# Kernel tuning notes

Hardware: AMD Instinct MI355X
Metric: run time of the kernel (lower is better)

Reference implementation:

```python
import jax, jax.numpy as jnp
import numpy as np

EPS = 1e-7  # keras.backend.epsilon()
CANONICAL_SIZE = 224.0
CANONICAL_LEVEL = 1.0
MIN_LEVEL, MAX_LEVEL = 0, 4


def _crop_and_resize(feat, boxes, crop_h, crop_w):
    """TF crop_and_resize (bilinear, extrapolation_value=0) for one image.
    feat: [H, W, C]; boxes: [N, 4] normalized (y1, x1, y2, x2).
    Returns [N, crop_h, crop_w, C]."""
    H, W, C = feat.shape
    hf = jnp.asarray(H - 1, feat.dtype)
    wf = jnp.asarray(W - 1, feat.dtype)
    y1, x1, y2, x2 = boxes[:, 0], boxes[:, 1], boxes[:, 2], boxes[:, 3]
    ty = jnp.arange(crop_h, dtype=feat.dtype) / (crop_h - 1)  # [ch]
    tx = jnp.arange(crop_w, dtype=feat.dtype) / (crop_w - 1)  # [cw]
    ys = (y1[:, None] + (y2 - y1)[:, None] * ty[None, :]) * hf  # [N, ch]
    xs = (x1[:, None] + (x2 - x1)[:, None] * tx[None, :]) * wf  # [N, cw]
    valid_y = (ys >= 0) & (ys <= hf)
    valid_x = (xs >= 0) & (xs <= wf)
    y0 = jnp.floor(ys)
    x0 = jnp.floor(xs)
    ly = ys - y0  # lerp weights [N, ch]
    lx = xs - x0  # [N, cw]
    y0i = jnp.clip(y0, 0, H - 1).astype(jnp.int32)
    y1i = jnp.clip(y0 + 1, 0, H - 1).astype(jnp.int32)
    x0i = jnp.clip(x0, 0, W - 1).astype(jnp.int32)
    x1i = jnp.clip(x0 + 1, 0, W - 1).astype(jnp.int32)
    # gather 4 corners -> [N, ch, cw, C]
    f00 = feat[y0i[:, :, None], x0i[:, None, :]]
    f01 = feat[y0i[:, :, None], x1i[:, None, :]]
    f10 = feat[y1i[:, :, None], x0i[:, None, :]]
    f11 = feat[y1i[:, :, None], x1i[:, None, :]]
    wy = ly[:, :, None, None]
    wx = lx[:, None, :, None]
    top = f00 + (f01 - f00) * wx
    bot = f10 + (f11 - f10) * wx
    out = top + (bot - top) * wy
    valid = (valid_y[:, :, None] & valid_x[:, None, :])[..., None]
    return jnp.where(valid, out, jnp.zeros((), feat.dtype))


def _map_to_level(boxes):
    w = boxes[:, 2] - boxes[:, 0]
    h = boxes[:, 3] - boxes[:, 1]
    size = jnp.sqrt(w * h)
    levels = jnp.floor(CANONICAL_LEVEL + jnp.log2(size / CANONICAL_SIZE + EPS))
    return jnp.clip(levels, MIN_LEVEL, MAX_LEVEL).astype(jnp.int32)


def roi_align(detections, fpn, top_k=1000, crop_size=(14, 14)):
    det = detections[0]                       # [N, 4+num_classes]
    scores = jnp.max(det[:, 4:], axis=1)      # [N]
    _, idx = jax.lax.top_k(scores, top_k)
    det = det[idx]                            # [K, 4+nc]
    levels = _map_to_level(det[:, :4])        # [K]
    # original concatenates level-0 rois, then level-1, ... == stable sort by level
    order = jnp.argsort(levels, stable=True)
    det = det[order]
    levels = levels[order]
    ch, cw = crop_size
    C = fpn[0].shape[-1]
    out = jnp.zeros((top_k, ch, cw, C), fpn[0].dtype)
    for i, f in enumerate(fpn):
        feat = f[0]                           # [H, W, C]
        H, W = feat.shape[0], feat.shape[1]
        hf = jnp.asarray(H - 1, feat.dtype)
        wf = jnp.asarray(W - 1, feat.dtype)
        boxes = jnp.stack([det[:, 1] / hf, det[:, 0] / wf,
                           det[:, 3] / hf, det[:, 2] / wf], axis=1)
        crops = _crop_and_resize(feat, boxes, ch, cw)
        out = jnp.where((levels == i)[:, None, None, None], crops, out)
    return out[None]                          # [1, K, ch, cw, C]


def setup_inputs() -> dict:
    key = jax.random.key(0)
    ks = jax.random.split(key, 10)
    N, NC = 5000, 80
    cx = jax.random.uniform(ks[0], (N,)) * 1024.0
    cy = jax.random.uniform(ks[1], (N,)) * 1024.0
    size = jnp.exp2(jax.random.uniform(ks[2], (N,)) * 5.0 + 5.0)   # 32..1024
    ar = jnp.exp2(jax.random.uniform(ks[3], (N,)) * 2.0 - 1.0)     # 0.5..2
    w = size * jnp.sqrt(ar)
    h = size / jnp.sqrt(ar)
    x1 = jnp.maximum(cx - w / 2, 0.0)
    y1 = jnp.maximum(cy - h / 2, 0.0)
    x2 = x1 + w
    y2 = y1 + h
    cls = jax.random.uniform(ks[4], (N, NC))
    detections = jnp.concatenate(
        [jnp.stack([x1, y1, x2, y2], axis=1), cls], axis=1)[None]  # [1,N,84]
    C = 256
    shapes = [256, 128, 64, 32, 16]
    fpn = {f"p{i}": jax.random.normal(ks[5 + i], (1, s, s, C), jnp.float32)
           for i, s in enumerate(shapes)}
    return {"detections": detections, **fpn}


def reference(detections, p0, p1, p2, p3, p4):
    return roi_align(detections, [p0, p1, p2, p3, p4],
                     top_k=1000, crop_size=(14, 14))
```

## Files before the change

kernel.cpp:

```cpp
#include <hip/hip_runtime.h>

#define NDET 5000
#define NCLS 80
#define DSTR 84
#define TOPK 1000
#define CROP 14
#define NPIX (CROP * CROP)
#define C    256

#define JCHUNK 250
#define ICHUNK 256

typedef float v4f __attribute__((ext_vector_type(4)));

__global__ void scores_kernel(const float* __restrict__ det, float* __restrict__ scores,
                              int* __restrict__ rank, int* __restrict__ lvl_all) {
    int i = blockIdx.x * blockDim.x + threadIdx.x;
    if (i >= NDET) return;
    const float* row = det + i * DSTR;
    const v4f* cls = (const v4f*)(row + 4);
    v4f m4 = cls[0];
    #pragma unroll
    for (int c = 1; c < NCLS / 4; ++c) {
        v4f v = cls[c];
        m4.x = fmaxf(m4.x, v.x); m4.y = fmaxf(m4.y, v.y);
        m4.z = fmaxf(m4.z, v.z); m4.w = fmaxf(m4.w, v.w);
    }
    scores[i] = fmaxf(fmaxf(m4.x, m4.y), fmaxf(m4.z, m4.w));
    rank[i] = 0;
    float w = row[2] - row[0];
    float h = row[3] - row[1];
    float sz = sqrtf(w * h);
    float lf = floorf(1.0f + log2f(sz / 224.0f + 1e-7f));
    lf = fminf(fmaxf(lf, 0.0f), 4.0f);
    lvl_all[i] = (int)lf;
}

__global__ __launch_bounds__(ICHUNK) void rank_kernel(const float* __restrict__ scores,
                                                      int* __restrict__ rank) {
    __shared__ float s[JCHUNK];
    int jbase = blockIdx.y * JCHUNK;
    for (int t = threadIdx.x; t < JCHUNK; t += blockDim.x) s[t] = scores[jbase + t];
    __syncthreads();
    int i = blockIdx.x * ICHUNK + threadIdx.x;
    if (i >= NDET) return;
    float my = scores[i];
    int r = 0;
    #pragma unroll 5
    for (int t = 0; t < JCHUNK; ++t) {
        float v = s[t];
        int j = jbase + t;
        r += (v > my) | ((v == my) & (j < i));
    }
    atomicAdd(&rank[i], r);
}

__global__ __launch_bounds__(1024) void order_kernel(const float* __restrict__ det,
                                                     const int* __restrict__ rank,
                                                     const int* __restrict__ lvl_all,
                                                     v4f* __restrict__ slot_params,
                                                     int* __restrict__ slot_level) {
    __shared__ int topk_idx_s[TOPK];
    __shared__ unsigned long long wave_tot[16];
    int r = threadIdx.x;
    for (int i = r; i < NDET; i += 1024) {
        int rk = rank[i];
        if (rk < TOPK) topk_idx_s[rk] = i;
    }
    __syncthreads();

    int di = 0, L = 0;
    unsigned long long key = 0;
    if (r < TOPK) {
        di = topk_idx_s[r];
        L = lvl_all[di];
        key = 1ULL << (12 * L);
    }
    unsigned long long incl = key;
    #pragma unroll
    for (int d = 1; d < 64; d <<= 1) {
        unsigned long long up = __shfl_up(incl, d, 64);
        if ((r & 63) >= d) incl += up;
    }
    int wave = r >> 6;
    if ((r & 63) == 63) wave_tot[wave] = incl;
    __syncthreads();
    unsigned long long waveoff = 0, total = 0;
    for (int w = 0; w < 16; ++w) {
        unsigned long long t = wave_tot[w];
        if (w < wave) waveoff += t;
        total += t;
    }
    if (r < TOPK) {
        unsigned long long excl = waveoff + incl - key;
        int base = 0;
        for (int l = 0; l < L; ++l) base += (int)((total >> (12 * l)) & 0xFFF);
        int within = (int)((excl >> (12 * L)) & 0xFFF);
        int pos = base + within;
        int H = 256 >> L;
        float hf = (float)(H - 1);
        const float* b = det + di * DSTR;
        float x1n = b[0] / hf, y1n = b[1] / hf;
        float x2n = b[2] / hf, y2n = b[3] / hf;
        v4f prm = {x1n, y1n, x2n - x1n, y2n - y1n};
        slot_params[pos] = prm;
        slot_level[pos] = L;
    }
}

__global__ __launch_bounds__(256) void crop_kernel(
    const float* __restrict__ p0, const float* __restrict__ p1,
    const float* __restrict__ p2, const float* __restrict__ p3,
    const float* __restrict__ p4,
    const v4f* __restrict__ slot_params, const int* __restrict__ slot_level,
    float* __restrict__ out)
{
    int wave = threadIdx.x >> 6;
    int lane = threadIdx.x & 63;
    int slot = blockIdx.x / 49;
    int p    = (blockIdx.x % 49) * 4 + wave;
    int py = p / CROP, px = p - py * CROP;

    int L = slot_level[slot];
    const float* feat;
    switch (L) {
        case 0:  feat = p0; break;
        case 1:  feat = p1; break;
        case 2:  feat = p2; break;
        case 3:  feat = p3; break;
        default: feat = p4; break;
    }
    int H = 256 >> L;
    float hf = (float)(H - 1);

    v4f prm = slot_params[slot];
    float ty = (float)py / 13.0f;
    float tx = (float)px / 13.0f;
    float ys = (prm.y + prm.w * ty) * hf;
    float xs = (prm.x + prm.z * tx) * hf;

    v4f* outp = (v4f*)(out + (size_t)(slot * NPIX + p) * C) + lane;

    bool valid = (ys >= 0.0f) & (ys <= hf) & (xs >= 0.0f) & (xs <= hf);
    if (!valid) {
        v4f z = {0.0f, 0.0f, 0.0f, 0.0f};
        *outp = z;
        return;
    }

    float y0f = floorf(ys), x0f = floorf(xs);
    float ly = ys - y0f,    lx = xs - x0f;
    int y0i = (int)fminf(fmaxf(y0f,        0.0f), hf);
    int y1i = (int)fminf(fmaxf(y0f + 1.0f, 0.0f), hf);
    int x0i = (int)fminf(fmaxf(x0f,        0.0f), hf);
    int x1i = (int)fminf(fmaxf(x0f + 1.0f, 0.0f), hf);

    v4f f00 = ((const v4f*)(feat + (size_t)(y0i * H + x0i) * C))[lane];
    v4f f01 = ((const v4f*)(feat + (size_t)(y0i * H + x1i) * C))[lane];
    v4f f10 = ((const v4f*)(feat + (size_t)(y1i * H + x0i) * C))[lane];
    v4f f11 = ((const v4f*)(feat + (size_t)(y1i * H + x1i) * C))[lane];

    v4f top = f00 + (f01 - f00) * lx;
    v4f bot = f10 + (f11 - f10) * lx;
    v4f o   = top + (bot - top) * ly;
    *outp = o;
}

extern "C" void kernel_launch(void* const* d_in, const int* in_sizes, int n_in,
                              void* d_out, int out_size, void* d_ws, size_t ws_size,
                              hipStream_t stream) {
    const float* det = (const float*)d_in[0];
    const float* p0  = (const float*)d_in[1];
    const float* p1  = (const float*)d_in[2];
    const float* p2  = (const float*)d_in[3];
    const float* p3  = (const float*)d_in[4];
    const float* p4  = (const float*)d_in[5];
    float* out = (float*)d_out;

    char* ws = (char*)d_ws;
    float* scores      = (float*)(ws + 0);
    int*   rank        = (int*)(ws + 20000);
    int*   lvl_all     = (int*)(ws + 40000);
    v4f*   slot_params = (v4f*)(ws + 60000);
    int*   slot_lvl    = (int*)(ws + 76000);

    scores_kernel<<<(NDET + 255) / 256, 256, 0, stream>>>(det, scores, rank, lvl_all);
    dim3 rg((NDET + ICHUNK - 1) / ICHUNK, NDET / JCHUNK);
    rank_kernel<<<rg, ICHUNK, 0, stream>>>(scores, rank);
    order_kernel<<<1, 1024, 0, stream>>>(det, rank, lvl_all, slot_params, slot_lvl);
    crop_kernel<<<TOPK * 49, 256, 0, stream>>>(p0, p1, p2, p3, p4,
                                               slot_params, slot_lvl, out);
}
```

Measured before the change: 281.9 us.

## Zero-fill output with nontemporal stores and crop only slots that can be in range

A grid-stride fill kernel now writes zeros over the whole output with nontemporal vector stores. The order kernel flags a slot as valid when its normalized top-left corner is at most 1. The crop kernel then runs one block per slot, returns early for unflagged slots, and loops over the 196 pixels with four waves, skipping pixels that fall out of range. The aim is to replace the 49k-block launch that mostly wrote zeros with one bandwidth-friendly fill plus much less gather work. The cost is that in-range slots are written twice, and the validity test assumes boxes with non-negative extent.

```diff
diff --git a/kernel.cpp b/kernel.cpp
--- a/kernel.cpp
+++ b/kernel.cpp
@@ -10,6 +10,7 @@
 
 #define JCHUNK 250
 #define ICHUNK 256
+#define FILL_BLOCKS 2048
 
 typedef float v4f __attribute__((ext_vector_type(4)));
 
@@ -55,11 +56,21 @@
     atomicAdd(&rank[i], r);
 }
 
+__global__ __launch_bounds__(256) void fill_kernel(v4f* __restrict__ out) {
+    const size_t total  = (size_t)TOPK * NPIX * (C / 4);
+    const size_t stride = (size_t)FILL_BLOCKS * 256;
+    size_t idx = (size_t)blockIdx.x * 256 + threadIdx.x;
+    v4f z = {0.0f, 0.0f, 0.0f, 0.0f};
+    for (; idx < total; idx += stride)
+        __builtin_nontemporal_store(z, out + idx);
+}
+
 __global__ __launch_bounds__(1024) void order_kernel(const float* __restrict__ det,
                                                      const int* __restrict__ rank,
                                                      const int* __restrict__ lvl_all,
                                                      v4f* __restrict__ slot_params,
-                                                     int* __restrict__ slot_level) {
+                                                     int* __restrict__ slot_level,
+                                                     int* __restrict__ slot_valid) {
     __shared__ int topk_idx_s[TOPK];
     __shared__ unsigned long long wave_tot[16];
     int r = threadIdx.x;
@@ -105,21 +116,22 @@
         v4f prm = {x1n, y1n, x2n - x1n, y2n - y1n};
         slot_params[pos] = prm;
         slot_level[pos] = L;
-    }
-}
-
-__global__ __launch_bounds__(256) void crop_kernel(
+        slot_valid[pos] = (x1n <= 1.0f) && (y1n <= 1.0f);
+    }
+}
+
+__global__ __launch_bounds__(256) void crop_sparse_kernel(
     const float* __restrict__ p0, const float* __restrict__ p1,
     const float* __restrict__ p2, const float* __restrict__ p3,
     const float* __restrict__ p4,
     const v4f* __restrict__ slot_params, const int* __restrict__ slot_level,
-    float* __restrict__ out)
+    const int* __restrict__ slot_valid, float* __restrict__ out)
 {
+    int slot = blockIdx.x;
+    if (!slot_valid[slot]) return;
+
     int wave = threadIdx.x >> 6;
     int lane = threadIdx.x & 63;
-    int slot = blockIdx.x / 49;
-    int p    = (blockIdx.x % 49) * 4 + wave;
-    int py = p / CROP, px = p - py * CROP;
 
     int L = slot_level[slot];
     const float* feat;
@@ -132,38 +144,40 @@
     }
     int H = 256 >> L;
     float hf = (float)(H - 1);
-
     v4f prm = slot_params[slot];
-    float ty = (float)py / 13.0f;
-    float tx = (float)px / 13.0f;
-    float ys = (prm.y + prm.w * ty) * hf;
-    float xs = (prm.x + prm.z * tx) * hf;
-
-    v4f* outp = (v4f*)(out + (size_t)(slot * NPIX + p) * C) + lane;
-
-    bool valid = (ys >= 0.0f) & (ys <= hf) & (xs >= 0.0f) & (xs <= hf);
-    if (!valid) {
-        v4f z = {0.0f, 0.0f, 0.0f, 0.0f};
-        *outp = z;
-        return;
-    }
-
-    float y0f = floorf(ys), x0f = floorf(xs);
-    float ly = ys - y0f,    lx = xs - x0f;
-    int y0i = (int)fminf(fmaxf(y0f,        0.0f), hf);
-    int y1i = (int)fminf(fmaxf(y0f + 1.0f, 0.0f), hf);
-    int x0i = (int)fminf(fmaxf(x0f,        0.0f), hf);
-    int x1i = (int)fminf(fmaxf(x0f + 1.0f, 0.0f), hf);
-
-    v4f f00 = ((const v4f*)(feat + (size_t)(y0i * H + x0i) * C))[lane];
-    v4f f01 = ((const v4f*)(feat + (size_t)(y0i * H + x1i) * C))[lane];
-    v4f f10 = ((const v4f*)(feat + (size_t)(y1i * H + x0i) * C))[lane];
-    v4f f11 = ((const v4f*)(feat + (size_t)(y1i * H + x1i) * C))[lane];
-
-    v4f top = f00 + (f01 - f00) * lx;
-    v4f bot = f10 + (f11 - f10) * lx;
-    v4f o   = top + (bot - top) * ly;
-    *outp = o;
+
+    const int cs = C / 4;
+    v4f* outbase = (v4f*)(out + (size_t)slot * NPIX * C) + lane;
+
+    #pragma unroll 7
+    for (int k = 0; k < 49; ++k) {
+        int p = k * 4 + wave;
+        int py = p / CROP, px = p - py * CROP;
+        float ty = (float)py / 13.0f;
+        float tx = (float)px / 13.0f;
+        float ys = (prm.y + prm.w * ty) * hf;
+        float xs = (prm.x + prm.z * tx) * hf;
+
+        bool valid = (ys >= 0.0f) & (ys <= hf) & (xs >= 0.0f) & (xs <= hf);
+        if (!valid) continue;
+
+        float y0f = floorf(ys), x0f = floorf(xs);
+        float ly = ys - y0f,    lx = xs - x0f;
+        int y0i = (int)fminf(fmaxf(y0f,        0.0f), hf);
+        int y1i = (int)fminf(fmaxf(y0f + 1.0f, 0.0f), hf);
+        int x0i = (int)fminf(fmaxf(x0f,        0.0f), hf);
+        int x1i = (int)fminf(fmaxf(x0f + 1.0f, 0.0f), hf);
+
+        v4f f00 = ((const v4f*)(feat + (size_t)(y0i * H + x0i) * C))[lane];
+        v4f f01 = ((const v4f*)(feat + (size_t)(y0i * H + x1i) * C))[lane];
+        v4f f10 = ((const v4f*)(feat + (size_t)(y1i * H + x0i) * C))[lane];
+        v4f f11 = ((const v4f*)(feat + (size_t)(y1i * H + x1i) * C))[lane];
+
+        v4f top = f00 + (f01 - f00) * lx;
+        v4f bot = f10 + (f11 - f10) * lx;
+        v4f o   = top + (bot - top) * ly;
+        outbase[p * cs] = o;
+    }
 }
 
 extern "C" void kernel_launch(void* const* d_in, const int* in_sizes, int n_in,
@@ -183,11 +197,14 @@
     int*   lvl_all     = (int*)(ws + 40000);
     v4f*   slot_params = (v4f*)(ws + 60000);
     int*   slot_lvl    = (int*)(ws + 76000);
+    int*   slot_valid  = (int*)(ws + 80000);
 
     scores_kernel<<<(NDET + 255) / 256, 256, 0, stream>>>(det, scores, rank, lvl_all);
     dim3 rg((NDET + ICHUNK - 1) / ICHUNK, NDET / JCHUNK);
     rank_kernel<<<rg, ICHUNK, 0, stream>>>(scores, rank);
-    order_kernel<<<1, 1024, 0, stream>>>(det, rank, lvl_all, slot_params, slot_lvl);
-    crop_kernel<<<TOPK * 49, 256, 0, stream>>>(p0, p1, p2, p3, p4,
-                                               slot_params, slot_lvl, out);
-}
+    fill_kernel<<<FILL_BLOCKS, 256, 0, stream>>>((v4f*)out);
+    order_kernel<<<1, 1024, 0, stream>>>(det, rank, lvl_all, slot_params, slot_lvl,
+                                         slot_valid);
+    crop_sparse_kernel<<<TOPK, 256, 0, stream>>>(p0, p1, p2, p3, p4,
+                                                 slot_params, slot_lvl, slot_valid, out);
+}
```

After: 326.2 us. +15.7%, slower.

## Fuse score computation into rank kernel and compute levels in order kernel

Applied to the files above, without the earlier changes.

Merges the scores and rank kernels into one 20-block kernel. Each block recomputes class-max scores for every chunk on the fly into shared memory and counts its own rank directly, with no atomics and no rank zeroing. Level mapping moves into the order kernel, computed only for the top-k boxes. This removes one launch and the global score and level buffers. In exchange the rank stage runs on only 20 blocks and every block recomputes all 5000 scores, so it has little parallelism.

```diff
diff --git a/kernel.cpp b/kernel.cpp
--- a/kernel.cpp
+++ b/kernel.cpp
@@ -8,56 +8,51 @@
 #define NPIX (CROP * CROP)
 #define C    256
 
-#define JCHUNK 250
-#define ICHUNK 256
+#define RCH 256
+#define NCH 20
 
 typedef float v4f __attribute__((ext_vector_type(4)));
 
-__global__ void scores_kernel(const float* __restrict__ det, float* __restrict__ scores,
-                              int* __restrict__ rank, int* __restrict__ lvl_all) {
-    int i = blockIdx.x * blockDim.x + threadIdx.x;
-    if (i >= NDET) return;
-    const float* row = det + i * DSTR;
-    const v4f* cls = (const v4f*)(row + 4);
-    v4f m4 = cls[0];
-    #pragma unroll
-    for (int c = 1; c < NCLS / 4; ++c) {
-        v4f v = cls[c];
-        m4.x = fmaxf(m4.x, v.x); m4.y = fmaxf(m4.y, v.y);
-        m4.z = fmaxf(m4.z, v.z); m4.w = fmaxf(m4.w, v.w);
+__global__ __launch_bounds__(RCH) void rank_fused_kernel(const float* __restrict__ det,
+                                                         int* __restrict__ rank) {
+    __shared__ float s[RCH];
+    int b = blockIdx.x;
+    int t = threadIdx.x;
+    int i = b * RCH + t;
+    float my = -__builtin_inff();
+    int r = 0;
+    for (int c = 0; c < NCH; ++c) {
+        int jc = b + c; if (jc >= NCH) jc -= NCH;
+        int row = jc * RCH + t;
+        float sc = -__builtin_inff();
+        if (row < NDET) {
+            const v4f* cls = (const v4f*)(det + row * DSTR + 4);
+            v4f m4 = cls[0];
+            #pragma unroll
+            for (int cc = 1; cc < NCLS / 4; ++cc) {
+                v4f v = cls[cc];
+                m4.x = fmaxf(m4.x, v.x); m4.y = fmaxf(m4.y, v.y);
+                m4.z = fmaxf(m4.z, v.z); m4.w = fmaxf(m4.w, v.w);
+            }
+            sc = fmaxf(fmaxf(m4.x, m4.y), fmaxf(m4.z, m4.w));
+        }
+        s[t] = sc;
+        __syncthreads();
+        if (c == 0) my = s[t];
+        int jbase = jc * RCH;
+        #pragma unroll 8
+        for (int u = 0; u < RCH; ++u) {
+            float v = s[u];
+            int j = jbase + u;
+            r += (v > my) | ((v == my) & (j < i));
+        }
+        __syncthreads();
     }
-    scores[i] = fmaxf(fmaxf(m4.x, m4.y), fmaxf(m4.z, m4.w));
-    rank[i] = 0;
-    float w = row[2] - row[0];
-    float h = row[3] - row[1];
-    float sz = sqrtf(w * h);
-    float lf = floorf(1.0f + log2f(sz / 224.0f + 1e-7f));
-    lf = fminf(fmaxf(lf, 0.0f), 4.0f);
-    lvl_all[i] = (int)lf;
-}
-
-__global__ __launch_bounds__(ICHUNK) void rank_kernel(const float* __restrict__ scores,
-                                                      int* __restrict__ rank) {
-    __shared__ float s[JCHUNK];
-    int jbase = blockIdx.y * JCHUNK;
-    for (int t = threadIdx.x; t < JCHUNK; t += blockDim.x) s[t] = scores[jbase + t];
-    __syncthreads();
-    int i = blockIdx.x * ICHUNK + threadIdx.x;
-    if (i >= NDET) return;
-    float my = scores[i];
-    int r = 0;
-    #pragma unroll 5
-    for (int t = 0; t < JCHUNK; ++t) {
-        float v = s[t];
-        int j = jbase + t;
-        r += (v > my) | ((v == my) & (j < i));
-    }
-    atomicAdd(&rank[i], r);
+    if (i < NDET) rank[i] = r;
 }
 
 __global__ __launch_bounds__(1024) void order_kernel(const float* __restrict__ det,
                                                      const int* __restrict__ rank,
-                                                     const int* __restrict__ lvl_all,
                                                      v4f* __restrict__ slot_params,
                                                      int* __restrict__ slot_level) {
     __shared__ int topk_idx_s[TOPK];
@@ -70,10 +65,17 @@
     __syncthreads();
 
     int di = 0, L = 0;
+    v4f box = {0.f, 0.f, 0.f, 0.f};
     unsigned long long key = 0;
     if (r < TOPK) {
         di = topk_idx_s[r];
-        L = lvl_all[di];
+        box = *(const v4f*)(det + di * DSTR);
+        float w = box.z - box.x;
+        float h = box.w - box.y;
+        float sz = sqrtf(w * h);
+        float lf = floorf(1.0f + log2f(sz / 224.0f + 1e-7f));
+        lf = fminf(fmaxf(lf, 0.0f), 4.0f);
+        L = (int)lf;
         key = 1ULL << (12 * L);
     }
     unsigned long long incl = key;
@@ -99,9 +101,8 @@
         int pos = base + within;
         int H = 256 >> L;
         float hf = (float)(H - 1);
-        const float* b = det + di * DSTR;
-        float x1n = b[0] / hf, y1n = b[1] / hf;
-        float x2n = b[2] / hf, y2n = b[3] / hf;
+        float x1n = box.x / hf, y1n = box.y / hf;
+        float x2n = box.z / hf, y2n = box.w / hf;
         v4f prm = {x1n, y1n, x2n - x1n, y2n - y1n};
         slot_params[pos] = prm;
         slot_level[pos] = L;
@@ -178,16 +179,12 @@
     float* out = (float*)d_out;
 
     char* ws = (char*)d_ws;
-    float* scores      = (float*)(ws + 0);
-    int*   rank        = (int*)(ws + 20000);
-    int*   lvl_all     = (int*)(ws + 40000);
-    v4f*   slot_params = (v4f*)(ws + 60000);
-    int*   slot_lvl    = (int*)(ws + 76000);
+    int*   rank        = (int*)(ws + 0);
+    v4f*   slot_params = (v4f*)(ws + 20032);
+    int*   slot_lvl    = (int*)(ws + 36032);
 
-    scores_kernel<<<(NDET + 255) / 256, 256, 0, stream>>>(det, scores, rank, lvl_all);
-    dim3 rg((NDET + ICHUNK - 1) / ICHUNK, NDET / JCHUNK);
-    rank_kernel<<<rg, ICHUNK, 0, stream>>>(scores, rank);
-    order_kernel<<<1, 1024, 0, stream>>>(det, rank, lvl_all, slot_params, slot_lvl);
+    rank_fused_kernel<<<NCH, RCH, 0, stream>>>(det, rank);
+    order_kernel<<<1, 1024, 0, stream>>>(det, rank, slot_params, slot_lvl);
     crop_kernel<<<TOPK * 49, 256, 0, stream>>>(p0, p1, p2, p3, p4,
                                                slot_params, slot_lvl, out);
 }
```

Result: slower. 427.9 us (+51.8%).
